# Performance work log

Hardware: AMD Instinct MI355X
Metric: run time of the kernel (lower is better)

The kernel has to match this reference:

```python
import jax, jax.numpy as jnp
import numpy as np

B, H, W, C = 32, 32, 32, 256
NUM_GROUPS = 32
EPS = 1e-5  # flax GroupNorm default


def setup_inputs() -> dict:
    key = jax.random.key(0)
    ks = jax.random.split(key, 6)
    s = C ** -0.5  # xavier-ish scale for [C,C] weights
    return {
        "x": jax.random.normal(ks[0], (B, H, W, C), dtype=jnp.float32),
        "gn_scale": jnp.ones((C,), jnp.float32),
        "gn_bias": jnp.zeros((C,), jnp.float32),
        "Wq": jax.random.normal(ks[1], (C, C), jnp.float32) * s,
        "bq": jnp.zeros((C,), jnp.float32),
        "Wk": jax.random.normal(ks[2], (C, C), jnp.float32) * s,
        "bk": jnp.zeros((C,), jnp.float32),
        "Wv": jax.random.normal(ks[3], (C, C), jnp.float32) * s,
        "bv": jnp.zeros((C,), jnp.float32),
        "Wo": jax.random.normal(ks[4], (C, C), jnp.float32) * s,
        "bo": jnp.zeros((C,), jnp.float32),
    }


def group_norm(x, scale, bias):
    b, h, w, c = x.shape
    g = NUM_GROUPS
    xg = x.reshape(b, h, w, g, c // g)
    mean = jnp.mean(xg, axis=(1, 2, 4), keepdims=True)
    var = jnp.var(xg, axis=(1, 2, 4), keepdims=True)
    xg = (xg - mean) * jax.lax.rsqrt(var + EPS)
    return xg.reshape(b, h, w, c) * scale + bias


def reference(x, gn_scale, gn_bias, Wq, bq, Wk, bk, Wv, bv, Wo, bo):
    b, h, w, c = x.shape
    ft = group_norm(x, gn_scale, gn_bias)
    q = jnp.tensordot(ft, Wq, 1) + bq  # [B,H,W,C]
    k = jnp.tensordot(ft, Wk, 1) + bk
    v = jnp.tensordot(ft, Wv, 1) + bv
    # full attention over spatial positions
    logits = jnp.einsum('bhwc,bHWc->bhwHW', q, k) * (c ** -0.5)
    attn_w = jax.nn.softmax(logits.reshape(b, h, w, h * w), axis=-1)
    attn_w = attn_w.reshape(b, h, w, h, w)
    attn = jnp.einsum('bhwHW,bHWc->bhwc', attn_w, v)
    attn = jnp.tensordot(attn, Wo, 1) + bo
    return x + attn
```

## Files before the change

kernel.cpp:

```cpp
#include <hip/hip_runtime.h>
#include <hip/hip_bf16.h>

#define EPSV  1e-5f
#define QSC   0.0625f

typedef __attribute__((ext_vector_type(8))) __bf16 bfrag;
typedef __attribute__((ext_vector_type(4))) float  f32x4;
typedef __attribute__((ext_vector_type(8))) short  s16x8;
typedef __attribute__((ext_vector_type(4))) short  s16x4;

static __device__ __forceinline__ short f2b(float f) {
    __hip_bfloat16 h = __float2bfloat16(f);
    return __builtin_bit_cast(short, h);
}

#define GLDS16(SRC, DST) __builtin_amdgcn_global_load_lds( \
    (__attribute__((address_space(1))) void*)(SRC),        \
    (__attribute__((address_space(3))) void*)(DST), 16, 0, 0)

__global__ __launch_bounds__(256) void gn_part_prep(const float* __restrict__ x,
                                                    float* __restrict__ part,
                                                    const float* __restrict__ wq,
                                                    const float* __restrict__ wk,
                                                    const float* __restrict__ wv,
                                                    const float* __restrict__ wo,
                                                    short* __restrict__ wt) {
    if (blockIdx.x >= 256) {
        const int bb = blockIdx.x - 256;
        const int z = bb >> 8;
        const int n = bb & 255;
        const int k = threadIdx.x;
        const float* w = (z == 0) ? wq : (z == 1) ? wk : (z == 2) ? wv : wo;
        wt[(z * 256 + n) * 256 + k] = f2b(w[k * 256 + n]);
        return;
    }
    const int b = blockIdx.x >> 3, ch = blockIdx.x & 7;
    const int t = threadIdx.x;
    const int c4 = t & 63;
    const int rr = t >> 6;
    float s1 = 0.f, s2 = 0.f;
    for (int i = 0; i < 32; ++i) {
        const int pos = ch * 128 + rr + (i << 2);
        const f32x4 v = *reinterpret_cast<const f32x4*>(x + (((b << 10) + pos) << 8) + (c4 << 2));
        s1 += v[0] + v[1] + v[2] + v[3];
        s2 += v[0]*v[0] + v[1]*v[1] + v[2]*v[2] + v[3]*v[3];
    }
    __shared__ float ls1[256], ls2[256];
    ls1[t] = s1; ls2[t] = s2;
    __syncthreads();
    if (t < 32) {
        float a1 = 0.f, a2 = 0.f;
        for (int r2 = 0; r2 < 4; ++r2)
            for (int e = 0; e < 2; ++e) {
                const int idx = r2 * 64 + t * 2 + e;
                a1 += ls1[idx]; a2 += ls2[idx];
            }
        part[((b * 8 + ch) * 32 + t) * 2 + 0] = a1;
        part[((b * 8 + ch) * 32 + t) * 2 + 1] = a2;
    }
}

__global__ __launch_bounds__(256) void qkv_gemm(const float* __restrict__ x,
                                                const float* __restrict__ part,
                                                const float* __restrict__ gns,
                                                const float* __restrict__ gnb,
                                                const short* __restrict__ wt,
                                                const float* __restrict__ bq,
                                                const float* __restrict__ bk,
                                                const float* __restrict__ bv,
                                                short* __restrict__ qo,
                                                short* __restrict__ ko,
                                                short* __restrict__ vtg) {
    __shared__ short At[64][264];
    __shared__ float gmean[32], grstd[32];
    __shared__ float sA[256], sB[256];

    const int t  = threadIdx.x;
    const int m0 = blockIdx.x * 64;
    const int b  = m0 >> 10;
    const int lane = t & 63, w = t >> 6;
    const int lr = lane & 15, lh = lane >> 4;

    if (t < 32) {
        float s1 = 0.f, s2 = 0.f;
        for (int ch = 0; ch < 8; ++ch) {
            s1 += part[((b * 8 + ch) * 32 + t) * 2 + 0];
            s2 += part[((b * 8 + ch) * 32 + t) * 2 + 1];
        }
        const float mean = s1 * (1.f / 8192.f);
        const float var  = s2 * (1.f / 8192.f) - mean * mean;
        gmean[t] = mean;
        grstd[t] = rsqrtf(var + EPSV);
    }
    __syncthreads();
    {
        const float a = grstd[t >> 3] * gns[t];
        sA[t] = a;
        sB[t] = gnb[t] - gmean[t >> 3] * a;
    }
    __syncthreads();

    {
        const int r = t >> 2, q4 = t & 3;
        const float* xrow = x + (m0 + r) * 256;
        for (int i = 0; i < 16; ++i) {
            const int c0 = (q4 + 4 * i) * 4;
            const f32x4 v  = *reinterpret_cast<const f32x4*>(xrow + c0);
            const f32x4 aa = *reinterpret_cast<const f32x4*>(&sA[c0]);
            const f32x4 bb = *reinterpret_cast<const f32x4*>(&sB[c0]);
            s16x4 o;
            for (int j = 0; j < 4; ++j) o[j] = f2b(v[j] * aa[j] + bb[j]);
            *reinterpret_cast<s16x4*>(&At[r][c0]) = o;
        }
    }
    __syncthreads();

    for (int z = 0; z < 3; ++z) {
        f32x4 acc[4][4];
        for (int mi = 0; mi < 4; ++mi)
            for (int ni = 0; ni < 4; ++ni) acc[mi][ni] = (f32x4){0.f, 0.f, 0.f, 0.f};
        const short* wz = wt + z * 65536 + (w * 64 + lr) * 256 + lh * 8;
#pragma unroll
        for (int kt = 0; kt < 8; ++kt) {
            bfrag bf[4];
#pragma unroll
            for (int ni = 0; ni < 4; ++ni)
                bf[ni] = *reinterpret_cast<const bfrag*>(wz + ni * 4096 + kt * 32);
            bfrag af[4];
#pragma unroll
            for (int mi = 0; mi < 4; ++mi)
                af[mi] = *reinterpret_cast<const bfrag*>(&At[mi * 16 + lr][kt * 32 + lh * 8]);
#pragma unroll
            for (int ni = 0; ni < 4; ++ni)
#pragma unroll
                for (int mi = 0; mi < 4; ++mi)
                    acc[mi][ni] = __builtin_amdgcn_mfma_f32_16x16x32_bf16(af[mi], bf[ni], acc[mi][ni], 0, 0, 0);
        }
        if (z == 2) {
            for (int ni = 0; ni < 4; ++ni) {
                const int col = w * 64 + ni * 16 + lr;
                const float bb = bv[col];
                for (int mi = 0; mi < 4; ++mi) {
                    const int pos = (m0 & 1023) + mi * 16 + lh * 4;
                    s16x4 ov;
                    for (int j = 0; j < 4; ++j) ov[j] = f2b(acc[mi][ni][j] + bb);
                    *reinterpret_cast<s16x4*>(&vtg[(((b << 8) + col) << 10) + pos]) = ov;
                }
            }
        } else {
            short* outp = (z == 0) ? qo : ko;
            const float* bias = (z == 0) ? bq : bk;
            const float s = (z == 0) ? QSC : 1.0f;
            for (int ni = 0; ni < 4; ++ni) {
                const int col = w * 64 + ni * 16 + lr;
                const float bsc = bias[col] * s;
                for (int mi = 0; mi < 4; ++mi) {
                    const int row = m0 + mi * 16 + lh * 4;
                    for (int j = 0; j < 4; ++j)
                        outp[(row + j) * 256 + col] = f2b(acc[mi][ni][j] * s + bsc);
                }
            }
        }
    }
}

__global__ __launch_bounds__(512) void attn_fused(const short* __restrict__ qq,
                                                  const short* __restrict__ kk,
                                                  const short* __restrict__ vt,
                                                  const short* __restrict__ wto,
                                                  const float* __restrict__ bo,
                                                  const float* __restrict__ x,
                                                  float* __restrict__ out) {
    __shared__ __align__(1024) short L[73728];

    int bid = blockIdx.x;
    bid = ((bid & 7) << 5) | (bid >> 3);
    const int b = bid >> 3, qt = bid & 7;
    const int t = threadIdx.x;
    const int w = t >> 6, lane = t & 63;
    const int lr = lane & 15, lh = lane >> 4;
    const int qr0 = qt * 128 + w * 16;
    const int sw = lr & 7;

    bfrag qf[8];
    {
        const short* qp = qq + (((b << 10) + qr0 + lr) << 8) + lh * 8;
#pragma unroll
        for (int ks = 0; ks < 8; ++ks)
            qf[ks] = *reinterpret_cast<const bfrag*>(qp + ks * 32);
    }

    const short* kbase = kk + ((long)b << 18);
    const short* vbase = vt + ((long)b << 18);
    short* plw = L + 65536 + (w << 10);

    auto stageK = [&](int kt_, int buf) {
#pragma unroll
        for (int t2 = 0; t2 < 4; ++t2) {
            const int rbase = w * 8 + t2 * 2;
            const int r  = rbase + (lane >> 5);
            const int gs = (lane & 31) ^ (r & 7);
            GLDS16(kbase + ((kt_ * 64 + r) << 8) + (gs << 3),
                   &L[buf * 16384 + (rbase << 8)]);
        }
    };
    auto stageV = [&](int kt_, int buf) {
#pragma unroll
        for (int t2 = 0; t2 < 4; ++t2) {
            const int rbase = w * 32 + t2 * 8;
            const int r  = rbase + (lane >> 3);
            const int gs = (lane & 7) ^ (r & 7);
            GLDS16(vbase + (r << 10) + kt_ * 64 + (gs << 3),
                   &L[32768 + buf * 16384 + (rbase << 6)]);
        }
    };

    f32x4 o[16];
#pragma unroll
    for (int ci = 0; ci < 16; ++ci) o[ci] = (f32x4){0.f, 0.f, 0.f, 0.f};
    float m = -3e38f, lsum = 0.f;

    stageK(0, 0); stageV(0, 0);

    for (int kt = 0; kt < 16; ++kt) {
        const int cur = kt & 1;
        __asm__ volatile("s_barrier" ::: "memory");
        if (kt < 15) {
            stageK(kt + 1, cur ^ 1);
            stageV(kt + 1, cur ^ 1);
            __asm__ volatile("s_waitcnt vmcnt(8)" ::: "memory");
        } else {
            __asm__ volatile("s_waitcnt vmcnt(0)" ::: "memory");
        }
        __asm__ volatile("s_barrier" ::: "memory");

        f32x4 sacc[4];
#pragma unroll
        for (int ni = 0; ni < 4; ++ni) sacc[ni] = (f32x4){0.f, 0.f, 0.f, 0.f};
        __builtin_amdgcn_s_setprio(1);
#pragma unroll
        for (int ks = 0; ks < 8; ++ks) {
#pragma unroll
            for (int ni = 0; ni < 4; ++ni) {
                const int row = ni * 16 + lr;
                const bfrag kf = *reinterpret_cast<const bfrag*>(
                    &L[cur * 16384 + (row << 8) + ((((ks << 2) + lh) ^ sw) << 3)]);
                sacc[ni] = __builtin_amdgcn_mfma_f32_16x16x32_bf16(kf, qf[ks], sacc[ni], 0, 0, 0);
            }
        }
        __builtin_amdgcn_s_setprio(0);

        float rm = fmaxf(fmaxf(sacc[0][0], sacc[0][1]), fmaxf(sacc[0][2], sacc[0][3]));
#pragma unroll
        for (int ni = 1; ni < 4; ++ni)
            rm = fmaxf(rm, fmaxf(fmaxf(sacc[ni][0], sacc[ni][1]),
                                 fmaxf(sacc[ni][2], sacc[ni][3])));
        rm = fmaxf(rm, __shfl_xor(rm, 16));
        rm = fmaxf(rm, __shfl_xor(rm, 32));

        const bool grow = __any(rm > m);
        float p[4][4];
        float rs = 0.f;
        if (grow) {
            const float mn = fmaxf(m, rm);
            const float sc = __expf(m - mn);
            m = mn;
#pragma unroll
            for (int ni = 0; ni < 4; ++ni)
#pragma unroll
                for (int r2 = 0; r2 < 4; ++r2) {
                    p[ni][r2] = __expf(sacc[ni][r2] - mn);
                    rs += p[ni][r2];
                }
            rs += __shfl_xor(rs, 16);
            rs += __shfl_xor(rs, 32);
            lsum = lsum * sc + rs;
            float scb[4];
#pragma unroll
            for (int j = 0; j < 4; ++j) scb[j] = __shfl(sc, lh * 4 + j);
#pragma unroll
            for (int ci = 0; ci < 16; ++ci)
#pragma unroll
                for (int j = 0; j < 4; ++j) o[ci][j] *= scb[j];
        } else {
#pragma unroll
            for (int ni = 0; ni < 4; ++ni)
#pragma unroll
                for (int r2 = 0; r2 < 4; ++r2) {
                    p[ni][r2] = __expf(sacc[ni][r2] - m);
                    rs += p[ni][r2];
                }
            rs += __shfl_xor(rs, 16);
            rs += __shfl_xor(rs, 32);
            lsum += rs;
        }

#pragma unroll
        for (int ni = 0; ni < 4; ++ni) {
            s16x4 pw;
#pragma unroll
            for (int r2 = 0; r2 < 4; ++r2) pw[r2] = f2b(p[ni][r2]);
            const int gc = (ni << 1) + (lh >> 1);
            const int ad = (lr << 6) + ((gc ^ sw) << 3) + ((lh & 1) << 2);
            *reinterpret_cast<s16x4*>(&plw[ad]) = pw;
        }
        const bfrag pa0 = *reinterpret_cast<const bfrag*>(
            &plw[(lr << 6) + ((lh ^ sw) << 3)]);
        const bfrag pa1 = *reinterpret_cast<const bfrag*>(
            &plw[(lr << 6) + (((4 + lh) ^ sw) << 3)]);

        __builtin_amdgcn_s_setprio(1);
#pragma unroll
        for (int ci = 0; ci < 16; ++ci) {
            const int row = (ci << 4) + lr;
            const bfrag vb0 = *reinterpret_cast<const bfrag*>(
                &L[32768 + cur * 16384 + (row << 6) + ((lh ^ sw) << 3)]);
            const bfrag vb1 = *reinterpret_cast<const bfrag*>(
                &L[32768 + cur * 16384 + (row << 6) + (((4 + lh) ^ sw) << 3)]);
            o[ci] = __builtin_amdgcn_mfma_f32_16x16x32_bf16(pa0, vb0, o[ci], 0, 0, 0);
            o[ci] = __builtin_amdgcn_mfma_f32_16x16x32_bf16(pa1, vb1, o[ci], 0, 0, 0);
        }
        __builtin_amdgcn_s_setprio(0);
    }

    float invb[4];
#pragma unroll
    for (int j = 0; j < 4; ++j) invb[j] = 1.0f / __shfl(lsum, lh * 4 + j);

    __syncthreads();

#pragma unroll
    for (int j = 0; j < 4; ++j) {
        const int rloc = w * 16 + lh * 4 + j;
#pragma unroll
        for (int ci = 0; ci < 16; ++ci)
            L[rloc * 264 + (ci << 4) + lr] = f2b(o[ci][j] * invb[j]);
    }
    __syncthreads();

    const int m0r = (b << 10) + qt * 128;
    f32x4 acc[8][2];
#pragma unroll
    for (int mi = 0; mi < 8; ++mi) {
        acc[mi][0] = (f32x4){0.f, 0.f, 0.f, 0.f};
        acc[mi][1] = (f32x4){0.f, 0.f, 0.f, 0.f};
    }
    const short* wz = wto + (w * 32 + lr) * 256 + lh * 8;
#pragma unroll
    for (int kt = 0; kt < 8; ++kt) {
        bfrag bf[2];
#pragma unroll
        for (int ni = 0; ni < 2; ++ni)
            bf[ni] = *reinterpret_cast<const bfrag*>(wz + ni * 4096 + kt * 32);
        bfrag af[8];
#pragma unroll
        for (int mi = 0; mi < 8; ++mi)
            af[mi] = *reinterpret_cast<const bfrag*>(
                &L[(mi * 16 + lr) * 264 + kt * 32 + lh * 8]);
#pragma unroll
        for (int ni = 0; ni < 2; ++ni)
#pragma unroll
            for (int mi = 0; mi < 8; ++mi)
                acc[mi][ni] = __builtin_amdgcn_mfma_f32_16x16x32_bf16(af[mi], bf[ni], acc[mi][ni], 0, 0, 0);
    }

#pragma unroll
    for (int ni = 0; ni < 2; ++ni) {
        const int col = w * 32 + ni * 16 + lr;
        const float bb = bo[col];
#pragma unroll
        for (int mi = 0; mi < 8; ++mi) {
            const int row = m0r + mi * 16 + lh * 4;
#pragma unroll
            for (int j = 0; j < 4; ++j) {
                const int idx = (row + j) * 256 + col;
                out[idx] = acc[mi][ni][j] + bb + x[idx];
            }
        }
    }
}

extern "C" void kernel_launch(void* const* d_in, const int* in_sizes, int n_in,
                              void* d_out, int out_size, void* d_ws, size_t ws_size,
                              hipStream_t stream) {
    const float* x   = (const float*)d_in[0];
    const float* gns = (const float*)d_in[1];
    const float* gnb = (const float*)d_in[2];
    const float* Wq  = (const float*)d_in[3];
    const float* bq  = (const float*)d_in[4];
    const float* Wk  = (const float*)d_in[5];
    const float* bk  = (const float*)d_in[6];
    const float* Wv  = (const float*)d_in[7];
    const float* bv  = (const float*)d_in[8];
    const float* Wo  = (const float*)d_in[9];
    const float* bo  = (const float*)d_in[10];
    float* out = (float*)d_out;

    char* ws = (char*)d_ws;
    short* wt   = (short*)(ws);
    float* part = (float*)(ws + 524288);
    const size_t MB16 = 16777216;
    short* qb  = (short*)(ws + (1 << 20));
    short* kb  = (short*)(ws + (1 << 20) + MB16);
    short* vtb = (short*)(ws + (1 << 20) + 2 * MB16);

    hipLaunchKernelGGL(gn_part_prep, dim3(1280), dim3(256), 0, stream,
                       x, part, Wq, Wk, Wv, Wo, wt);
    hipLaunchKernelGGL(qkv_gemm, dim3(512), dim3(256), 0, stream,
                       x, part, gns, gnb, wt, bq, bk, bv, qb, kb, vtb);
    hipLaunchKernelGGL(attn_fused, dim3(256), dim3(512), 0, stream,
                       qb, kb, vtb, wt + 3 * 65536, bo, x, out);
}
```

Before: 130.7 us.

## Merge three kernels into one cooperative persistent kernel with grid syncs

Replaces the three separate launches (group-norm stats plus weight transpose, QKV GEMM, fused attention) with a single cooperative kernel of 256 blocks that separates the phases with grid.sync. The goal is to remove launch gaps and per-kernel tail effects. Each phase is remapped onto 512-thread blocks: the QKV GEMM now handles 128 rows per block in two halves, and the weight transpose writes 4 elements per thread. The residual x is apparently preloaded into registers before the output store. In exchange it adds grid-barrier cost and restricts the grid to what can be co-resident, so the early phases run with fewer, larger blocks than before.

```diff
diff --git a/kernel.cpp b/kernel.cpp
--- a/kernel.cpp
+++ b/kernel.cpp
@@ -1,5 +1,8 @@
 #include <hip/hip_runtime.h>
 #include <hip/hip_bf16.h>
+#include <hip/hip_cooperative_groups.h>
+
+namespace cg = cooperative_groups;
 
 #define EPSV  1e-5f
 #define QSC   0.0625f
@@ -18,363 +21,375 @@
     (__attribute__((address_space(1))) void*)(SRC),        \
     (__attribute__((address_space(3))) void*)(DST), 16, 0, 0)
 
-__global__ __launch_bounds__(256) void gn_part_prep(const float* __restrict__ x,
-                                                    float* __restrict__ part,
-                                                    const float* __restrict__ wq,
-                                                    const float* __restrict__ wk,
-                                                    const float* __restrict__ wv,
-                                                    const float* __restrict__ wo,
-                                                    short* __restrict__ wt) {
-    if (blockIdx.x >= 256) {
-        const int bb = blockIdx.x - 256;
-        const int z = bb >> 8;
-        const int n = bb & 255;
-        const int k = threadIdx.x;
-        const float* w = (z == 0) ? wq : (z == 1) ? wk : (z == 2) ? wv : wo;
-        wt[(z * 256 + n) * 256 + k] = f2b(w[k * 256 + n]);
-        return;
+__global__ __launch_bounds__(512) void mega(
+    const float* __restrict__ x,
+    const float* __restrict__ gns, const float* __restrict__ gnb,
+    const float* __restrict__ wq,  const float* __restrict__ bq,
+    const float* __restrict__ wk,  const float* __restrict__ bk,
+    const float* __restrict__ wv,  const float* __restrict__ bv,
+    const float* __restrict__ wo,  const float* __restrict__ bo,
+    float* __restrict__ part, short* __restrict__ wt,
+    short* __restrict__ qb, short* __restrict__ kb, short* __restrict__ vtb,
+    float* __restrict__ out)
+{
+    __shared__ __align__(1024) short L[73728];
+    cg::grid_group grid = cg::this_grid();
+
+    const int bid  = blockIdx.x;
+    const int t    = threadIdx.x;
+    const int w    = t >> 6, lane = t & 63;
+    const int lr   = lane & 15, lh = lane >> 4;
+
+    {
+        if (t < 256) {
+            const int b = bid >> 3, ch = bid & 7;
+            const int c4 = t & 63, rr = t >> 6;
+            float s1 = 0.f, s2 = 0.f;
+            for (int i = 0; i < 32; ++i) {
+                const int pos = ch * 128 + rr + (i << 2);
+                const f32x4 v = *reinterpret_cast<const f32x4*>(
+                    x + (((b << 10) + pos) << 8) + (c4 << 2));
+                s1 += v[0] + v[1] + v[2] + v[3];
+                s2 += v[0]*v[0] + v[1]*v[1] + v[2]*v[2] + v[3]*v[3];
+            }
+            float* ls1 = (float*)L;
+            float* ls2 = (float*)L + 256;
+            ls1[t] = s1; ls2[t] = s2;
+        } else {
+            const int u  = (bid << 8) + (t - 256);
+            const int z  = u >> 14;
+            const int r  = u & 16383;
+            const int n  = r >> 6;
+            const int k4 = (r & 63) << 2;
+            const float* wsrc = (z == 0) ? wq : (z == 1) ? wk : (z == 2) ? wv : wo;
+            s16x4 o;
+            for (int e = 0; e < 4; ++e) o[e] = f2b(wsrc[(k4 + e) * 256 + n]);
+            *reinterpret_cast<s16x4*>(&wt[((z * 256 + n) << 8) + k4]) = o;
+        }
+        __syncthreads();
+        if (t < 32) {
+            float* ls1 = (float*)L;
+            float* ls2 = (float*)L + 256;
+            float a1 = 0.f, a2 = 0.f;
+            for (int r2 = 0; r2 < 4; ++r2)
+                for (int e = 0; e < 2; ++e) {
+                    const int idx = r2 * 64 + t * 2 + e;
+                    a1 += ls1[idx]; a2 += ls2[idx];
+                }
+            const int b = bid >> 3, ch = bid & 7;
+            part[((b * 8 + ch) * 32 + t) * 2 + 0] = a1;
+            part[((b * 8 + ch) * 32 + t) * 2 + 1] = a2;
+        }
     }
-    const int b = blockIdx.x >> 3, ch = blockIdx.x & 7;
-    const int t = threadIdx.x;
-    const int c4 = t & 63;
-    const int rr = t >> 6;
-    float s1 = 0.f, s2 = 0.f;
-    for (int i = 0; i < 32; ++i) {
-        const int pos = ch * 128 + rr + (i << 2);
-        const f32x4 v = *reinterpret_cast<const f32x4*>(x + (((b << 10) + pos) << 8) + (c4 << 2));
-        s1 += v[0] + v[1] + v[2] + v[3];
-        s2 += v[0]*v[0] + v[1]*v[1] + v[2]*v[2] + v[3]*v[3];
+    grid.sync();
+
+    {
+        const int half = w >> 2, w4 = w & 3;
+        const int b    = bid >> 3;
+        const int m0   = (bid << 7) + (half << 6);
+        float* gm = (float*)(L + 33792);
+        float* gr = gm + 32;
+        float* sA = gr + 32;
+        float* sB = sA + 256;
+
+        if (t < 32) {
+            float s1 = 0.f, s2 = 0.f;
+            for (int ch = 0; ch < 8; ++ch) {
+                s1 += part[((b * 8 + ch) * 32 + t) * 2 + 0];
+                s2 += part[((b * 8 + ch) * 32 + t) * 2 + 1];
+            }
+            const float mean = s1 * (1.f / 8192.f);
+            const float var  = s2 * (1.f / 8192.f) - mean * mean;
+            gm[t] = mean;
+            gr[t] = rsqrtf(var + EPSV);
+        }
+        __syncthreads();
+        if (t < 256) {
+            const float a = gr[t >> 3] * gns[t];
+            sA[t] = a;
+            sB[t] = gnb[t] - gm[t >> 3] * a;
+        }
+        __syncthreads();
+
+        {
+            const int hh = t >> 8;
+            const int tt = t & 255;
+            const int r = tt >> 2, q4 = tt & 3;
+            short* Ath = L + hh * 16896;
+            const float* xrow = x + ((bid << 7) + (hh << 6) + r) * 256;
+            for (int i = 0; i < 16; ++i) {
+                const int c0 = (q4 + 4 * i) * 4;
+                const f32x4 v  = *reinterpret_cast<const f32x4*>(xrow + c0);
+                const f32x4 aa = *reinterpret_cast<const f32x4*>(&sA[c0]);
+                const f32x4 bb = *reinterpret_cast<const f32x4*>(&sB[c0]);
+                s16x4 o;
+                for (int j = 0; j < 4; ++j) o[j] = f2b(v[j] * aa[j] + bb[j]);
+                *reinterpret_cast<s16x4*>(&Ath[r * 264 + c0]) = o;
+            }
+        }
+        __syncthreads();
+
+        short* At = L + half * 16896;
+        for (int z = 0; z < 3; ++z) {
+            f32x4 acc[4][4];
+            for (int mi = 0; mi < 4; ++mi)
+                for (int ni = 0; ni < 4; ++ni) acc[mi][ni] = (f32x4){0.f, 0.f, 0.f, 0.f};
+            const short* wz = wt + z * 65536 + (w4 * 64 + lr) * 256 + lh * 8;
+#pragma unroll
+            for (int kt = 0; kt < 8; ++kt) {
+                bfrag bf[4];
+#pragma unroll
+                for (int ni = 0; ni < 4; ++ni)
+                    bf[ni] = *reinterpret_cast<const bfrag*>(wz + ni * 4096 + kt * 32);
+                bfrag af[4];
+#pragma unroll
+                for (int mi = 0; mi < 4; ++mi)
+                    af[mi] = *reinterpret_cast<const bfrag*>(&At[(mi * 16 + lr) * 264 + kt * 32 + lh * 8]);
+#pragma unroll
+                for (int ni = 0; ni < 4; ++ni)
+#pragma unroll
+                    for (int mi = 0; mi < 4; ++mi)
+                        acc[mi][ni] = __builtin_amdgcn_mfma_f32_16x16x32_bf16(af[mi], bf[ni], acc[mi][ni], 0, 0, 0);
+            }
+            if (z == 2) {
+                for (int ni = 0; ni < 4; ++ni) {
+                    const int col = w4 * 64 + ni * 16 + lr;
+                    const float bb = bv[col];
+                    for (int mi = 0; mi < 4; ++mi) {
+                        const int pos = (m0 & 1023) + mi * 16 + lh * 4;
+                        s16x4 ov;
+                        for (int j = 0; j < 4; ++j) ov[j] = f2b(acc[mi][ni][j] + bb);
+                        *reinterpret_cast<s16x4*>(&vtb[(((b << 8) + col) << 10) + pos]) = ov;
+                    }
+                }
+            } else {
+                short* outp = (z == 0) ? qb : kb;
+                const float* bias = (z == 0) ? bq : bk;
+                const float s = (z == 0) ? QSC : 1.0f;
+                for (int ni = 0; ni < 4; ++ni) {
+                    const int col = w4 * 64 + ni * 16 + lr;
+                    const float bsc = bias[col] * s;
+                    for (int mi = 0; mi < 4; ++mi) {
+                        const int row = m0 + mi * 16 + lh * 4;
+                        for (int j = 0; j < 4; ++j)
+                            outp[(row + j) * 256 + col] = f2b(acc[mi][ni][j] * s + bsc);
+                    }
+                }
+            }
+        }
     }
-    __shared__ float ls1[256], ls2[256];
-    ls1[t] = s1; ls2[t] = s2;
-    __syncthreads();
-    if (t < 32) {
-        float a1 = 0.f, a2 = 0.f;
-        for (int r2 = 0; r2 < 4; ++r2)
-            for (int e = 0; e < 2; ++e) {
-                const int idx = r2 * 64 + t * 2 + e;
-                a1 += ls1[idx]; a2 += ls2[idx];
-            }
-        part[((b * 8 + ch) * 32 + t) * 2 + 0] = a1;
-        part[((b * 8 + ch) * 32 + t) * 2 + 1] = a2;
-    }
-}
-
-__global__ __launch_bounds__(256) void qkv_gemm(const float* __restrict__ x,
-                                                const float* __restrict__ part,
-                                                const float* __restrict__ gns,
-                                                const float* __restrict__ gnb,
-                                                const short* __restrict__ wt,
-                                                const float* __restrict__ bq,
-                                                const float* __restrict__ bk,
-                                                const float* __restrict__ bv,
-                                                short* __restrict__ qo,
-                                                short* __restrict__ ko,
-                                                short* __restrict__ vtg) {
-    __shared__ short At[64][264];
-    __shared__ float gmean[32], grstd[32];
-    __shared__ float sA[256], sB[256];
-
-    const int t  = threadIdx.x;
-    const int m0 = blockIdx.x * 64;
-    const int b  = m0 >> 10;
-    const int lane = t & 63, w = t >> 6;
-    const int lr = lane & 15, lh = lane >> 4;
-
-    if (t < 32) {
-        float s1 = 0.f, s2 = 0.f;
-        for (int ch = 0; ch < 8; ++ch) {
-            s1 += part[((b * 8 + ch) * 32 + t) * 2 + 0];
-            s2 += part[((b * 8 + ch) * 32 + t) * 2 + 1];
-        }
-        const float mean = s1 * (1.f / 8192.f);
-        const float var  = s2 * (1.f / 8192.f) - mean * mean;
-        gmean[t] = mean;
-        grstd[t] = rsqrtf(var + EPSV);
-    }
-    __syncthreads();
+    grid.sync();
+
     {
-        const float a = grstd[t >> 3] * gns[t];
-        sA[t] = a;
-        sB[t] = gnb[t] - gmean[t >> 3] * a;
-    }
-    __syncthreads();
-
-    {
-        const int r = t >> 2, q4 = t & 3;
-        const float* xrow = x + (m0 + r) * 256;
-        for (int i = 0; i < 16; ++i) {
-            const int c0 = (q4 + 4 * i) * 4;
-            const f32x4 v  = *reinterpret_cast<const f32x4*>(xrow + c0);
-            const f32x4 aa = *reinterpret_cast<const f32x4*>(&sA[c0]);
-            const f32x4 bb = *reinterpret_cast<const f32x4*>(&sB[c0]);
-            s16x4 o;
-            for (int j = 0; j < 4; ++j) o[j] = f2b(v[j] * aa[j] + bb[j]);
-            *reinterpret_cast<s16x4*>(&At[r][c0]) = o;
-        }
-    }
-    __syncthreads();
-
-    for (int z = 0; z < 3; ++z) {
-        f32x4 acc[4][4];
-        for (int mi = 0; mi < 4; ++mi)
-            for (int ni = 0; ni < 4; ++ni) acc[mi][ni] = (f32x4){0.f, 0.f, 0.f, 0.f};
-        const short* wz = wt + z * 65536 + (w * 64 + lr) * 256 + lh * 8;
+        int bid3 = ((bid & 7) << 5) | (bid >> 3);
+        const int b = bid3 >> 3, qt = bid3 & 7;
+        const int qr0 = qt * 128 + w * 16;
+        const int sw = lr & 7;
+
+        bfrag qf[8];
+        {
+            const short* qp = qb + (((b << 10) + qr0 + lr) << 8) + lh * 8;
+#pragma unroll
+            for (int ks = 0; ks < 8; ++ks)
+                qf[ks] = *reinterpret_cast<const bfrag*>(qp + ks * 32);
+        }
+
+        const short* kbase = kb + ((long)b << 18);
+        const short* vbase = vtb + ((long)b << 18);
+        short* plw = L + 65536 + (w << 10);
+
+        auto stageK = [&](int kt_, int buf) {
+#pragma unroll
+            for (int t2 = 0; t2 < 4; ++t2) {
+                const int rbase = w * 8 + t2 * 2;
+                const int r  = rbase + (lane >> 5);
+                const int gs = (lane & 31) ^ (r & 7);
+                GLDS16(kbase + ((kt_ * 64 + r) << 8) + (gs << 3),
+                       &L[buf * 16384 + (rbase << 8)]);
+            }
+        };
+        auto stageV = [&](int kt_, int buf) {
+#pragma unroll
+            for (int t2 = 0; t2 < 4; ++t2) {
+                const int rbase = w * 32 + t2 * 8;
+                const int r  = rbase + (lane >> 3);
+                const int gs = (lane & 7) ^ (r & 7);
+                GLDS16(vbase + (r << 10) + kt_ * 64 + (gs << 3),
+                       &L[32768 + buf * 16384 + (rbase << 6)]);
+            }
+        };
+
+        f32x4 o[16];
+#pragma unroll
+        for (int ci = 0; ci < 16; ++ci) o[ci] = (f32x4){0.f, 0.f, 0.f, 0.f};
+        float m = -3e38f, lsum = 0.f;
+
+        stageK(0, 0); stageV(0, 0);
+
+        for (int kt = 0; kt < 16; ++kt) {
+            const int cur = kt & 1;
+            __asm__ volatile("s_barrier" ::: "memory");
+            if (kt < 15) {
+                stageK(kt + 1, cur ^ 1);
+                stageV(kt + 1, cur ^ 1);
+                __asm__ volatile("s_waitcnt vmcnt(8)" ::: "memory");
+            } else {
+                __asm__ volatile("s_waitcnt vmcnt(0)" ::: "memory");
+            }
+            __asm__ volatile("s_barrier" ::: "memory");
+
+            f32x4 sacc[4];
+#pragma unroll
+            for (int ni = 0; ni < 4; ++ni) sacc[ni] = (f32x4){0.f, 0.f, 0.f, 0.f};
+            __builtin_amdgcn_s_setprio(1);
+#pragma unroll
+            for (int ks = 0; ks < 8; ++ks) {
+#pragma unroll
+                for (int ni = 0; ni < 4; ++ni) {
+                    const int row = ni * 16 + lr;
+                    const bfrag kf = *reinterpret_cast<const bfrag*>(
+                        &L[cur * 16384 + (row << 8) + ((((ks << 2) + lh) ^ sw) << 3)]);
+                    sacc[ni] = __builtin_amdgcn_mfma_f32_16x16x32_bf16(kf, qf[ks], sacc[ni], 0, 0, 0);
+                }
+            }
+            __builtin_amdgcn_s_setprio(0);
+
+            float rm = fmaxf(fmaxf(sacc[0][0], sacc[0][1]), fmaxf(sacc[0][2], sacc[0][3]));
+#pragma unroll
+            for (int ni = 1; ni < 4; ++ni)
+                rm = fmaxf(rm, fmaxf(fmaxf(sacc[ni][0], sacc[ni][1]),
+                                     fmaxf(sacc[ni][2], sacc[ni][3])));
+            rm = fmaxf(rm, __shfl_xor(rm, 16));
+            rm = fmaxf(rm, __shfl_xor(rm, 32));
+
+            const bool grow = __any(rm > m);
+            float p[4][4];
+            float rs = 0.f;
+            if (grow) {
+                const float mn = fmaxf(m, rm);
+                const float sc = __expf(m - mn);
+                m = mn;
+#pragma unroll
+                for (int ni = 0; ni < 4; ++ni)
+#pragma unroll
+                    for (int r2 = 0; r2 < 4; ++r2) {
+                        p[ni][r2] = __expf(sacc[ni][r2] - mn);
+                        rs += p[ni][r2];
+                    }
+                rs += __shfl_xor(rs, 16);
+                rs += __shfl_xor(rs, 32);
+                lsum = lsum * sc + rs;
+                float scb[4];
+#pragma unroll
+                for (int j = 0; j < 4; ++j) scb[j] = __shfl(sc, lh * 4 + j);
+#pragma unroll
+                for (int ci = 0; ci < 16; ++ci)
+#pragma unroll
+                    for (int j = 0; j < 4; ++j) o[ci][j] *= scb[j];
+            } else {
+#pragma unroll
+                for (int ni = 0; ni < 4; ++ni)
+#pragma unroll
+                    for (int r2 = 0; r2 < 4; ++r2) {
+                        p[ni][r2] = __expf(sacc[ni][r2] - m);
+                        rs += p[ni][r2];
+                    }
+                rs += __shfl_xor(rs, 16);
+                rs += __shfl_xor(rs, 32);
+                lsum += rs;
+            }
+
+#pragma unroll
+            for (int ni = 0; ni < 4; ++ni) {
+                s16x4 pw;
+#pragma unroll
+                for (int r2 = 0; r2 < 4; ++r2) pw[r2] = f2b(p[ni][r2]);
+                const int gc = (ni << 1) + (lh >> 1);
+                const int ad = (lr << 6) + ((gc ^ sw) << 3) + ((lh & 1) << 2);
+                *reinterpret_cast<s16x4*>(&plw[ad]) = pw;
+            }
+            const bfrag pa0 = *reinterpret_cast<const bfrag*>(
+                &plw[(lr << 6) + ((lh ^ sw) << 3)]);
+            const bfrag pa1 = *reinterpret_cast<const bfrag*>(
+                &plw[(lr << 6) + (((4 + lh) ^ sw) << 3)]);
+
+            __builtin_amdgcn_s_setprio(1);
+#pragma unroll
+            for (int ci = 0; ci < 16; ++ci) {
+                const int row = (ci << 4) + lr;
+                const bfrag vb0 = *reinterpret_cast<const bfrag*>(
+                    &L[32768 + cur * 16384 + (row << 6) + ((lh ^ sw) << 3)]);
+                const bfrag vb1 = *reinterpret_cast<const bfrag*>(
+                    &L[32768 + cur * 16384 + (row << 6) + (((4 + lh) ^ sw) << 3)]);
+                o[ci] = __builtin_amdgcn_mfma_f32_16x16x32_bf16(pa0, vb0, o[ci], 0, 0, 0);
+                o[ci] = __builtin_amdgcn_mfma_f32_16x16x32_bf16(pa1, vb1, o[ci], 0, 0, 0);
+            }
+            __builtin_amdgcn_s_setprio(0);
+        }
+
+        float invb[4];
+#pragma unroll
+        for (int j = 0; j < 4; ++j) invb[j] = 1.0f / __shfl(lsum, lh * 4 + j);
+
+        __syncthreads();
+
+        const int m0r = (b << 10) + qt * 128;
+        float xr[2][8][4];
+#pragma unroll
+        for (int ni = 0; ni < 2; ++ni) {
+            const int col = w * 32 + ni * 16 + lr;
+#pragma unroll
+            for (int mi = 0; mi < 8; ++mi)
+#pragma unroll
+                for (int j = 0; j < 4; ++j)
+                    xr[ni][mi][j] = x[(m0r + mi * 16 + lh * 4 + j) * 256 + col];
+        }
+
+#pragma unroll
+        for (int j = 0; j < 4; ++j) {
+            const int rloc = w * 16 + lh * 4 + j;
+#pragma unroll
+            for (int ci = 0; ci < 16; ++ci)
+                L[rloc * 264 + (ci << 4) + lr] = f2b(o[ci][j] * invb[j]);
+        }
+        __syncthreads();
+
+        const short* wto = wt + 3 * 65536;
+        f32x4 acc[8][2];
+#pragma unroll
+        for (int mi = 0; mi < 8; ++mi) {
+            acc[mi][0] = (f32x4){0.f, 0.f, 0.f, 0.f};
+            acc[mi][1] = (f32x4){0.f, 0.f, 0.f, 0.f};
+        }
+        const short* wz = wto + (w * 32 + lr) * 256 + lh * 8;
 #pragma unroll
         for (int kt = 0; kt < 8; ++kt) {
-            bfrag bf[4];
-#pragma unroll
-            for (int ni = 0; ni < 4; ++ni)
+            bfrag bf[2];
+#pragma unroll
+            for (int ni = 0; ni < 2; ++ni)
                 bf[ni] = *reinterpret_cast<const bfrag*>(wz + ni * 4096 + kt * 32);
-            bfrag af[4];
-#pragma unroll
-            for (int mi = 0; mi < 4; ++mi)
-                af[mi] = *reinterpret_cast<const bfrag*>(&At[mi * 16 + lr][kt * 32 + lh * 8]);
-#pragma unroll
-            for (int ni = 0; ni < 4; ++ni)
-#pragma unroll
-                for (int mi = 0; mi < 4; ++mi)
+            bfrag af[8];
+#pragma unroll
+            for (int mi = 0; mi < 8; ++mi)
+                af[mi] = *reinterpret_cast<const bfrag*>(
+                    &L[(mi * 16 + lr) * 264 + kt * 32 + lh * 8]);
+#pragma unroll
+            for (int ni = 0; ni < 2; ++ni)
+#pragma unroll
+                for (int mi = 0; mi < 8; ++mi)
                     acc[mi][ni] = __builtin_amdgcn_mfma_f32_16x16x32_bf16(af[mi], bf[ni], acc[mi][ni], 0, 0, 0);
         }
-        if (z == 2) {
-            for (int ni = 0; ni < 4; ++ni) {
-                const int col = w * 64 + ni * 16 + lr;
-                const float bb = bv[col];
-                for (int mi = 0; mi < 4; ++mi) {
-                    const int pos = (m0 & 1023) + mi * 16 + lh * 4;
-                    s16x4 ov;
-                    for (int j = 0; j < 4; ++j) ov[j] = f2b(acc[mi][ni][j] + bb);
-                    *reinterpret_cast<s16x4*>(&vtg[(((b << 8) + col) << 10) + pos]) = ov;
-                }
-            }
-        } else {
-            short* outp = (z == 0) ? qo : ko;
-            const float* bias = (z == 0) ? bq : bk;
-            const float s = (z == 0) ? QSC : 1.0f;
-            for (int ni = 0; ni < 4; ++ni) {
-                const int col = w * 64 + ni * 16 + lr;
-                const float bsc = bias[col] * s;
-                for (int mi = 0; mi < 4; ++mi) {
-                    const int row = m0 + mi * 16 + lh * 4;
-                    for (int j = 0; j < 4; ++j)
-                        outp[(row + j) * 256 + col] = f2b(acc[mi][ni][j] * s + bsc);
-                }
-            }
-        }
-    }
-}
-
-__global__ __launch_bounds__(512) void attn_fused(const short* __restrict__ qq,
-                                                  const short* __restrict__ kk,
-                                                  const short* __restrict__ vt,
-                                                  const short* __restrict__ wto,
-                                                  const float* __restrict__ bo,
-                                                  const float* __restrict__ x,
-                                                  float* __restrict__ out) {
-    __shared__ __align__(1024) short L[73728];
-
-    int bid = blockIdx.x;
-    bid = ((bid & 7) << 5) | (bid >> 3);
-    const int b = bid >> 3, qt = bid & 7;
-    const int t = threadIdx.x;
-    const int w = t >> 6, lane = t & 63;
-    const int lr = lane & 15, lh = lane >> 4;
-    const int qr0 = qt * 128 + w * 16;
-    const int sw = lr & 7;
-
-    bfrag qf[8];
-    {
-        const short* qp = qq + (((b << 10) + qr0 + lr) << 8) + lh * 8;
-#pragma unroll
-        for (int ks = 0; ks < 8; ++ks)
-            qf[ks] = *reinterpret_cast<const bfrag*>(qp + ks * 32);
-    }
-
-    const short* kbase = kk + ((long)b << 18);
-    const short* vbase = vt + ((long)b << 18);
-    short* plw = L + 65536 + (w << 10);
-
-    auto stageK = [&](int kt_, int buf) {
-#pragma unroll
-        for (int t2 = 0; t2 < 4; ++t2) {
-            const int rbase = w * 8 + t2 * 2;
-            const int r  = rbase + (lane >> 5);
-            const int gs = (lane & 31) ^ (r & 7);
-            GLDS16(kbase + ((kt_ * 64 + r) << 8) + (gs << 3),
-                   &L[buf * 16384 + (rbase << 8)]);
-        }
-    };
-    auto stageV = [&](int kt_, int buf) {
-#pragma unroll
-        for (int t2 = 0; t2 < 4; ++t2) {
-            const int rbase = w * 32 + t2 * 8;
-            const int r  = rbase + (lane >> 3);
-            const int gs = (lane & 7) ^ (r & 7);
-            GLDS16(vbase + (r << 10) + kt_ * 64 + (gs << 3),
-                   &L[32768 + buf * 16384 + (rbase << 6)]);
-        }
-    };
-
-    f32x4 o[16];
-#pragma unroll
-    for (int ci = 0; ci < 16; ++ci) o[ci] = (f32x4){0.f, 0.f, 0.f, 0.f};
-    float m = -3e38f, lsum = 0.f;
-
-    stageK(0, 0); stageV(0, 0);
-
-    for (int kt = 0; kt < 16; ++kt) {
-        const int cur = kt & 1;
-        __asm__ volatile("s_barrier" ::: "memory");
-        if (kt < 15) {
-            stageK(kt + 1, cur ^ 1);
-            stageV(kt + 1, cur ^ 1);
-            __asm__ volatile("s_waitcnt vmcnt(8)" ::: "memory");
-        } else {
-            __asm__ volatile("s_waitcnt vmcnt(0)" ::: "memory");
-        }
-        __asm__ volatile("s_barrier" ::: "memory");
-
-        f32x4 sacc[4];
-#pragma unroll
-        for (int ni = 0; ni < 4; ++ni) sacc[ni] = (f32x4){0.f, 0.f, 0.f, 0.f};
-        __builtin_amdgcn_s_setprio(1);
-#pragma unroll
-        for (int ks = 0; ks < 8; ++ks) {
-#pragma unroll
-            for (int ni = 0; ni < 4; ++ni) {
-                const int row = ni * 16 + lr;
-                const bfrag kf = *reinterpret_cast<const bfrag*>(
-                    &L[cur * 16384 + (row << 8) + ((((ks << 2) + lh) ^ sw) << 3)]);
-                sacc[ni] = __builtin_amdgcn_mfma_f32_16x16x32_bf16(kf, qf[ks], sacc[ni], 0, 0, 0);
-            }
-        }
-        __builtin_amdgcn_s_setprio(0);
-
-        float rm = fmaxf(fmaxf(sacc[0][0], sacc[0][1]), fmaxf(sacc[0][2], sacc[0][3]));
-#pragma unroll
-        for (int ni = 1; ni < 4; ++ni)
-            rm = fmaxf(rm, fmaxf(fmaxf(sacc[ni][0], sacc[ni][1]),
-                                 fmaxf(sacc[ni][2], sacc[ni][3])));
-        rm = fmaxf(rm, __shfl_xor(rm, 16));
-        rm = fmaxf(rm, __shfl_xor(rm, 32));
-
-        const bool grow = __any(rm > m);
-        float p[4][4];
-        float rs = 0.f;
-        if (grow) {
-            const float mn = fmaxf(m, rm);
-            const float sc = __expf(m - mn);
-            m = mn;
-#pragma unroll
-            for (int ni = 0; ni < 4; ++ni)
-#pragma unroll
-                for (int r2 = 0; r2 < 4; ++r2) {
-                    p[ni][r2] = __expf(sacc[ni][r2] - mn);
-                    rs += p[ni][r2];
-                }
-            rs += __shfl_xor(rs, 16);
-            rs += __shfl_xor(rs, 32);
-            lsum = lsum * sc + rs;
-            float scb[4];
-#pragma unroll
-            for (int j = 0; j < 4; ++j) scb[j] = __shfl(sc, lh * 4 + j);
-#pragma unroll
-            for (int ci = 0; ci < 16; ++ci)
-#pragma unroll
-                for (int j = 0; j < 4; ++j) o[ci][j] *= scb[j];
-        } else {
-#pragma unroll
-            for (int ni = 0; ni < 4; ++ni)
-#pragma unroll
-                for (int r2 = 0; r2 < 4; ++r2) {
-                    p[ni][r2] = __expf(sacc[ni][r2] - m);
-                    rs += p[ni][r2];
-                }
-            rs += __shfl_xor(rs, 16);
-            rs += __shfl_xor(rs, 32);
-            lsum += rs;
-        }
-
-#pragma unroll
-        for (int ni = 0; ni < 4; ++ni) {
-            s16x4 pw;
-#pragma unroll
-            for (int r2 = 0; r2 < 4; ++r2) pw[r2] = f2b(p[ni][r2]);
-            const int gc = (ni << 1) + (lh >> 1);
-            const int ad = (lr << 6) + ((gc ^ sw) << 3) + ((lh & 1) << 2);
-            *reinterpret_cast<s16x4*>(&plw[ad]) = pw;
-        }
-        const bfrag pa0 = *reinterpret_cast<const bfrag*>(
-            &plw[(lr << 6) + ((lh ^ sw) << 3)]);
-        const bfrag pa1 = *reinterpret_cast<const bfrag*>(
-            &plw[(lr << 6) + (((4 + lh) ^ sw) << 3)]);
-
-        __builtin_amdgcn_s_setprio(1);
-#pragma unroll
-        for (int ci = 0; ci < 16; ++ci) {
-            const int row = (ci << 4) + lr;
-            const bfrag vb0 = *reinterpret_cast<const bfrag*>(
-                &L[32768 + cur * 16384 + (row << 6) + ((lh ^ sw) << 3)]);
-            const bfrag vb1 = *reinterpret_cast<const bfrag*>(
-                &L[32768 + cur * 16384 + (row << 6) + (((4 + lh) ^ sw) << 3)]);
-            o[ci] = __builtin_amdgcn_mfma_f32_16x16x32_bf16(pa0, vb0, o[ci], 0, 0, 0);
-            o[ci] = __builtin_amdgcn_mfma_f32_16x16x32_bf16(pa1, vb1, o[ci], 0, 0, 0);
-        }
-        __builtin_amdgcn_s_setprio(0);
-    }
-
-    float invb[4];
-#pragma unroll
-    for (int j = 0; j < 4; ++j) invb[j] = 1.0f / __shfl(lsum, lh * 4 + j);
-
-    __syncthreads();
-
-#pragma unroll
-    for (int j = 0; j < 4; ++j) {
-        const int rloc = w * 16 + lh * 4 + j;
-#pragma unroll
-        for (int ci = 0; ci < 16; ++ci)
-            L[rloc * 264 + (ci << 4) + lr] = f2b(o[ci][j] * invb[j]);
-    }
-    __syncthreads();
-
-    const int m0r = (b << 10) + qt * 128;
-    f32x4 acc[8][2];
-#pragma unroll
-    for (int mi = 0; mi < 8; ++mi) {
-        acc[mi][0] = (f32x4){0.f, 0.f, 0.f, 0.f};
-        acc[mi][1] = (f32x4){0.f, 0.f, 0.f, 0.f};
-    }
-    const short* wz = wto + (w * 32 + lr) * 256 + lh * 8;
-#pragma unroll
-    for (int kt = 0; kt < 8; ++kt) {
-        bfrag bf[2];
-#pragma unroll
-        for (int ni = 0; ni < 2; ++ni)
-            bf[ni] = *reinterpret_cast<const bfrag*>(wz + ni * 4096 + kt * 32);
-        bfrag af[8];
-#pragma unroll
-        for (int mi = 0; mi < 8; ++mi)
-            af[mi] = *reinterpret_cast<const bfrag*>(
-                &L[(mi * 16 + lr) * 264 + kt * 32 + lh * 8]);
-#pragma unroll
-        for (int ni = 0; ni < 2; ++ni)
-#pragma unroll
-            for (int mi = 0; mi < 8; ++mi)
-                acc[mi][ni] = __builtin_amdgcn_mfma_f32_16x16x32_bf16(af[mi], bf[ni], acc[mi][ni], 0, 0, 0);
-    }
-
-#pragma unroll
-    for (int ni = 0; ni < 2; ++ni) {
-        const int col = w * 32 + ni * 16 + lr;
-        const float bb = bo[col];
-#pragma unroll
-        for (int mi = 0; mi < 8; ++mi) {
-            const int row = m0r + mi * 16 + lh * 4;
-#pragma unroll
-            for (int j = 0; j < 4; ++j) {
-                const int idx = (row + j) * 256 + col;
-                out[idx] = acc[mi][ni][j] + bb + x[idx];
+
+#pragma unroll
+        for (int ni = 0; ni < 2; ++ni) {
+            const int col = w * 32 + ni * 16 + lr;
+            const float bb = bo[col];
+#pragma unroll
+            for (int mi = 0; mi < 8; ++mi) {
+                const int row = m0r + mi * 16 + lh * 4;
+#pragma unroll
+                for (int j = 0; j < 4; ++j)
+                    out[(row + j) * 256 + col] = acc[mi][ni][j] + bb + xr[ni][mi][j];
             }
         }
     }
@@ -404,10 +419,12 @@
     short* kb  = (short*)(ws + (1 << 20) + MB16);
     short* vtb = (short*)(ws + (1 << 20) + 2 * MB16);
 
-    hipLaunchKernelGGL(gn_part_prep, dim3(1280), dim3(256), 0, stream,
-                       x, part, Wq, Wk, Wv, Wo, wt);
-    hipLaunchKernelGGL(qkv_gemm, dim3(512), dim3(256), 0, stream,
-                       x, part, gns, gnb, wt, bq, bk, bv, qb, kb, vtb);
-    hipLaunchKernelGGL(attn_fused, dim3(256), dim3(512), 0, stream,
-                       qb, kb, vtb, wt + 3 * 65536, bo, x, out);
+    void* args[] = {
+        (void*)&x, (void*)&gns, (void*)&gnb,
+        (void*)&Wq, (void*)&bq, (void*)&Wk, (void*)&bk,
+        (void*)&Wv, (void*)&bv, (void*)&Wo, (void*)&bo,
+        (void*)&part, (void*)&wt, (void*)&qb, (void*)&kb, (void*)&vtb,
+        (void*)&out
+    };
+    hipLaunchCooperativeKernel((void*)mega, dim3(256), dim3(512), args, 0, stream);
 }
```

Result: slower. 224.0 us (+71.3%).
